# Kernel optimization log

Measured on AMD Instinct MI355X. Metric: run time of the kernel, lower is better.

Reference implementation:

```python
import jax, jax.numpy as jnp
import numpy as np

E, H_HEADS, WS = 512, 16, 8
HEAD_D = E // H_HEADS
LN_EPS = 1e-5


def layernorm(x, g, b):
    mu = jnp.mean(x, axis=-1, keepdims=True)
    var = jnp.mean((x - mu) ** 2, axis=-1, keepdims=True)
    return (x - mu) / jnp.sqrt(var + LN_EPS) * g + b


def setup_inputs() -> dict:
    key = jax.random.key(0)
    ks = jax.random.split(key, 10)
    s = 0.02
    return {
        "x": jax.random.normal(ks[0], (4, 4096, E), jnp.float32),
        "in_proj_w": jax.random.normal(ks[1], (3 * E, E), jnp.float32) * s,
        "in_proj_b": jnp.zeros((3 * E,), jnp.float32),
        "out_w": jax.random.normal(ks[2], (E, E), jnp.float32) * s,
        "out_b": jnp.zeros((E,), jnp.float32),
        "ln1_g": jnp.ones((E,), jnp.float32),
        "ln1_b": jnp.zeros((E,), jnp.float32),
        "w1": jax.random.normal(ks[3], (4 * E, E), jnp.float32) * s,
        "b1": jnp.zeros((4 * E,), jnp.float32),
        "w2": jax.random.normal(ks[4], (E, 4 * E), jnp.float32) * s,
        "b2": jnp.zeros((E,), jnp.float32),
        "ln2_g": jnp.ones((E,), jnp.float32),
        "ln2_b": jnp.zeros((E,), jnp.float32),
        "num_patches_h": 64,
        "num_patches_w": 64,
    }


def reference(x, in_proj_w, in_proj_b, out_w, out_b, ln1_g, ln1_b,
              w1, b1, w2, b2, ln2_g, ln2_b, num_patches_h, num_patches_w):
    B, P, _ = x.shape
    Hp, Wp = num_patches_h, num_patches_w  # 64 divisible by WS -> no padding branch
    nwh, nww = Hp // WS, Wp // WS
    # window partition: (B, Hp, Wp, E) -> (B*nW, WS*WS, E)
    xw = x.reshape(B, nwh, WS, nww, WS, E).transpose(0, 1, 3, 2, 4, 5)
    xw = xw.reshape(B * nwh * nww, WS * WS, E)
    # nn.MultiheadAttention default batch_first=False: axis0 is SEQ (L=B*nW),
    # axis1 is BATCH (N=WS*WS). Reproduce that literal semantics.
    L, N = xw.shape[0], xw.shape[1]
    qkv = xw @ in_proj_w.T + in_proj_b          # (L, N, 3E)
    q, k, v = jnp.split(qkv, 3, axis=-1)
    qh = q.reshape(L, N, H_HEADS, HEAD_D)
    kh = k.reshape(L, N, H_HEADS, HEAD_D)
    vh = v.reshape(L, N, H_HEADS, HEAD_D)
    scale = 1.0 / np.sqrt(HEAD_D)
    scores = jnp.einsum('lnhd,mnhd->nhlm', qh, kh) * scale  # (N, h, L, L)
    attn = jax.nn.softmax(scores, axis=-1)
    o = jnp.einsum('nhlm,mnhd->lnhd', attn, vh).reshape(L, N, E)
    attn_out = o @ out_w.T + out_b
    y = layernorm(xw + attn_out, ln1_g, ln1_b)
    ffn = jax.nn.gelu(y @ w1.T + b1, approximate=False) @ w2.T + b2
    y = layernorm(y + ffn, ln2_g, ln2_b)
    # window unpartition
    y = y.reshape(B, nwh, nww, WS, WS, E).transpose(0, 1, 3, 2, 4, 5)
    return y.reshape(B, Hp * Wp, E)[:, :P, :]
```

## Files before the change

### kernel.cpp

```cpp
#include <hip/hip_runtime.h>
#include <cmath>


typedef _Float16 half8 __attribute__((ext_vector_type(8)));
typedef _Float16 half4v __attribute__((ext_vector_type(4)));
typedef float f32x4 __attribute__((ext_vector_type(4)));

#define GLOBAL_AS(p) ((const __attribute__((address_space(1))) void*)(p))
#define LDS_AS(p) ((__attribute__((address_space(3))) void*)(p))

__device__ __forceinline__ void gload_lds16(const _Float16* g, _Float16* l) {
  __builtin_amdgcn_global_load_lds(GLOBAL_AS(g), LDS_AS(l), 16, 0, 0);
}

__device__ __forceinline__ float wave_sum(float v) {
#pragma unroll
  for (int off = 32; off > 0; off >>= 1) v += __shfl_xor(v, off, 64);
  return v;
}

__device__ __forceinline__ float gelu_fast(float x) {
  const float y = 1.5957691216057308f * (x + 0.044715f * x * x * x);
  const float e = __expf(y);
  const float t = 1.0f - 2.0f / (e + 1.0f);
  return 0.5f * x * (1.0f + t);
}

__global__ __launch_bounds__(256) void pre_kernel(
    const float* __restrict__ x, _Float16* __restrict__ xw,
    const float* __restrict__ s0, _Float16* __restrict__ d0,
    const float* __restrict__ s1, _Float16* __restrict__ d1,
    const float* __restrict__ s2, _Float16* __restrict__ d2,
    const float* __restrict__ s3, _Float16* __restrict__ d3) {
  int b = blockIdx.x;
  if (b < 4096) {
    const int idx = b * 256 + threadIdx.x;
    const int t = idx >> 6;
    const int e0 = (idx & 63) << 3;
    const int l = t >> 6, n = t & 63;
    const int bb = l >> 6, wh = (l >> 3) & 7, ww = l & 7;
    const int pi = n >> 3, pj = n & 7;
    const int xrow = (bb * 4096 + (wh * 8 + pi) * 64 + (ww * 8 + pj)) * 512;
    const float4 a = *(const float4*)&x[xrow + e0];
    const float4 c = *(const float4*)&x[xrow + e0 + 4];
    half8 o;
    o[0] = (_Float16)a.x; o[1] = (_Float16)a.y; o[2] = (_Float16)a.z; o[3] = (_Float16)a.w;
    o[4] = (_Float16)c.x; o[5] = (_Float16)c.y; o[6] = (_Float16)c.z; o[7] = (_Float16)c.w;
    *(half8*)&xw[t * 512 + e0] = o;
    return;
  }
  b -= 4096;
  const float* s; _Float16* d;
  if (b < 768) { s = s0; d = d0; }
  else if (b < 1024) { s = s1; d = d1; b -= 768; }
  else if (b < 2048) { s = s2; d = d2; b -= 1024; }
  else { s = s3; d = d3; b -= 2048; }
  const int i = (b * 256 + threadIdx.x) * 4;
  const float4 v = *(const float4*)&s[i];
  half4v o;
  o[0] = (_Float16)v.x; o[1] = (_Float16)v.y; o[2] = (_Float16)v.z; o[3] = (_Float16)v.w;
  *(half4v*)&d[i] = o;
}

template <int EPI, int K, int BN, int MREP>
__global__ __launch_bounds__(256, 4) void gemml_kernel(
    const _Float16* __restrict__ A, const _Float16* __restrict__ B,
    const float* __restrict__ bias, _Float16* __restrict__ C, int N) {
  constexpr int NT = K / 64;
  constexpr int NWR = (BN == 128) ? 2 : 4;
  constexpr int BM = NWR * MREP * 16;
  constexpr int TA = BM * 64;
  constexpr int TB = BN * 64;
  __shared__ _Float16 L[TA + TB];

  const int tid = threadIdx.x, lane = tid & 63, wave = tid >> 6;
  const int wr = (BN == 128) ? (wave >> 1) : wave;
  const int wc = (BN == 128) ? (wave & 1) : 0;
  const int lr = lane & 15, g = lane >> 4;

  const int nbn = N / BN;
  const int cpx = gridDim.x >> 3;
  const int wg = (blockIdx.x & 7) * cpx + (blockIdx.x >> 3);
  const int bm = wg / nbn, bn = wg % nbn;

  const int scol = ((lane & 7) ^ (lane >> 3)) << 3;
  const int srow = lane >> 3;
  const _Float16* aS = A + (size_t)(bm * BM + wave * 8 + srow) * K + scol;
  const _Float16* bS = B + (size_t)(bn * BN + wave * 8 + srow) * K + scol;

  const int sw0 = ((g ^ (lr & 7)) << 3);
  const int sw1 = (((4 + g) ^ (lr & 7)) << 3);
  int arow[MREP], brow[4];
#pragma unroll
  for (int m = 0; m < MREP; ++m) arow[m] = (wr * (MREP * 16) + m * 16 + lr) * 64;
#pragma unroll
  for (int n = 0; n < 4; ++n) brow[n] = TA + (wc * 64 + n * 16 + lr) * 64;

  f32x4 acc[MREP][4] = {};

#pragma unroll 8
  for (int t = 0; t < NT; ++t) {
    const int koff = t * 64;
#pragma unroll
    for (int i = 0; i < BM / 32; ++i)
      gload_lds16(aS + (size_t)(i * 32) * K + koff, &L[(i * 32 + wave * 8) * 64]);
#pragma unroll
    for (int i = 0; i < BN / 32; ++i)
      gload_lds16(bS + (size_t)(i * 32) * K + koff, &L[TA + (i * 32 + wave * 8) * 64]);
    __syncthreads();
    half8 af[MREP], bf[4];
#pragma unroll
    for (int m = 0; m < MREP; ++m) af[m] = *(const half8*)&L[arow[m] + sw0];
#pragma unroll
    for (int n = 0; n < 4; ++n) bf[n] = *(const half8*)&L[brow[n] + sw0];
    __builtin_amdgcn_s_setprio(1);
#pragma unroll
    for (int m = 0; m < MREP; ++m)
#pragma unroll
      for (int n = 0; n < 4; ++n)
        acc[m][n] = __builtin_amdgcn_mfma_f32_16x16x32_f16(af[m], bf[n], acc[m][n], 0, 0, 0);
    __builtin_amdgcn_s_setprio(0);
#pragma unroll
    for (int m = 0; m < MREP; ++m) af[m] = *(const half8*)&L[arow[m] + sw1];
#pragma unroll
    for (int n = 0; n < 4; ++n) bf[n] = *(const half8*)&L[brow[n] + sw1];
    __builtin_amdgcn_s_setprio(1);
#pragma unroll
    for (int m = 0; m < MREP; ++m)
#pragma unroll
      for (int n = 0; n < 4; ++n)
        acc[m][n] = __builtin_amdgcn_mfma_f32_16x16x32_f16(af[m], bf[n], acc[m][n], 0, 0, 0);
    __builtin_amdgcn_s_setprio(0);
    __syncthreads();
  }

  float bsv[4];
#pragma unroll
  for (int n = 0; n < 4; ++n) bsv[n] = bias[bn * BN + wc * 64 + n * 16 + lr];
  _Float16* Lc = &L[0] + wave * (MREP * 16 * 64);
#pragma unroll
  for (int m = 0; m < MREP; ++m)
#pragma unroll
    for (int n = 0; n < 4; ++n)
#pragma unroll
      for (int r = 0; r < 4; ++r) {
        float v = acc[m][n][r] + bsv[n];
        if (EPI == 1) v = gelu_fast(v);
        const int row = m * 16 + g * 4 + r;
        const int col = n * 16 + lr;
        Lc[row * 64 + (col ^ ((row & 7) << 3))] = (_Float16)v;
      }
  asm volatile("s_waitcnt lgkmcnt(0)" ::: "memory");
  const int rrow = lane >> 3, slot = lane & 7;
  const int growb = bm * BM + wr * (MREP * 16);
  const int gcol = bn * BN + wc * 64 + slot * 8;
#pragma unroll
  for (int blk = 0; blk < MREP * 2; ++blk) {
    const int row = blk * 8 + rrow;
    const half8 vv = *(const half8*)&Lc[row * 64 + ((slot ^ (row & 7)) << 3)];
    *(half8*)&C[(size_t)(growb + row) * N + gcol] = vv;
  }
}

__global__ __launch_bounds__(256) void attn_kernel(const _Float16* __restrict__ qkv,
                                                   _Float16* __restrict__ o_out) {
  const int n = blockIdx.x & 63;
  const int h = blockIdx.x >> 6;
  __shared__ _Float16 Ksh[256 * 40];
  __shared__ _Float16 Vt[32 * 264];
  __shared__ _Float16 Pw[4 * 64 * 72];
  const int tid = threadIdx.x;
  const int wq = tid >> 6, lane = tid & 63;
  const int lr = lane & 15, g = lane >> 4;
  const int hq = h * 32;

#pragma unroll
  for (int pass = 0; pass < 4; ++pass) {
    const int e = pass * 2048 + tid * 8;
    const int m = e >> 5, d = e & 31;
    const int base = (m * 64 + n) * 1536 + hq;
    const half8 k8 = *(const half8*)&qkv[base + 512 + d];
    const half8 v8 = *(const half8*)&qkv[base + 1024 + d];
    *(half8*)&Ksh[m * 40 + d] = k8;
#pragma unroll
    for (int j = 0; j < 8; ++j) Vt[(d + j) * 264 + m] = v8[j];
  }
  half8 qf[4];
#pragma unroll
  for (int qt = 0; qt < 4; ++qt) {
    const int qg = wq * 64 + qt * 16 + lr;
    qf[qt] = *(const half8*)&qkv[(qg * 64 + n) * 1536 + hq + g * 8];
  }
  __syncthreads();

  f32x4 o[4][2] = {};
  float den[4] = {0.f, 0.f, 0.f, 0.f};
  const float scale = 0.17677669529663687f;
  _Float16* P = &Pw[wq * (64 * 72)];

  for (int it = 0; it < 4; ++it) {
    const int k0 = it * 64;
#pragma unroll
    for (int qt = 0; qt < 4; ++qt) {
#pragma unroll
      for (int kt = 0; kt < 4; ++kt) {
        const half8 kf = *(const half8*)&Ksh[(k0 + kt * 16 + lr) * 40 + g * 8];
        const f32x4 z = {0.f, 0.f, 0.f, 0.f};
        f32x4 st = __builtin_amdgcn_mfma_f32_16x16x32_f16(kf, qf[qt], z, 0, 0, 0);
        const float p0 = __expf(st[0] * scale);
        const float p1 = __expf(st[1] * scale);
        const float p2 = __expf(st[2] * scale);
        const float p3 = __expf(st[3] * scale);
        den[qt] += (p0 + p1) + (p2 + p3);
        half4v w;
        w[0] = (_Float16)p0; w[1] = (_Float16)p1;
        w[2] = (_Float16)p2; w[3] = (_Float16)p3;
        *(half4v*)&P[(qt * 16 + lr) * 72 + kt * 16 + g * 4] = w;
      }
    }
    __syncthreads();
#pragma unroll
    for (int qt = 0; qt < 4; ++qt) {
#pragma unroll
      for (int ks = 0; ks < 2; ++ks) {
        const half8 pf = *(const half8*)&P[(qt * 16 + lr) * 72 + ks * 32 + g * 8];
#pragma unroll
        for (int dt = 0; dt < 2; ++dt) {
          const half8 vf = *(const half8*)&Vt[(dt * 16 + lr) * 264 + k0 + ks * 32 + g * 8];
          o[qt][dt] = __builtin_amdgcn_mfma_f32_16x16x32_f16(pf, vf, o[qt][dt], 0, 0, 0);
        }
      }
    }
    __syncthreads();
  }

#pragma unroll
  for (int qt = 0; qt < 4; ++qt) {
    float dq = den[qt];
    dq += __shfl_xor(dq, 16);
    dq += __shfl_xor(dq, 32);
    const float inv = 1.0f / dq;
#pragma unroll
    for (int r = 0; r < 4; ++r) {
      const float invr = __shfl(inv, g * 4 + r);
      const int qg = wq * 64 + qt * 16 + g * 4 + r;
      const int obase = (qg * 64 + n) * 512 + hq;
#pragma unroll
      for (int dt = 0; dt < 2; ++dt)
        o_out[obase + dt * 16 + lr] = (_Float16)(o[qt][dt][r] * invr);
    }
  }
}

template <int FINAL>
__global__ __launch_bounds__(256) void ln_kernel(
    const float* __restrict__ res32, const _Float16* __restrict__ res16,
    const _Float16* __restrict__ add16,
    const float* __restrict__ g, const float* __restrict__ b,
    float* __restrict__ out32, _Float16* __restrict__ out16) {
  const int t = blockIdx.x * 4 + (threadIdx.x >> 6);
  const int lane = threadIdx.x & 63;
  const int e0 = lane << 3;
  const int l = t >> 6, n = t & 63;
  const int bb = l >> 6, wh = (l >> 3) & 7, ww = l & 7;
  const int pi = n >> 3, pj = n & 7;
  const int xrow = (bb * 4096 + (wh * 8 + pi) * 64 + (ww * 8 + pj)) * 512;
  const int trow = t * 512;
  const half8 a8 = *(const half8*)&add16[trow + e0];
  float v[8];
  if (FINAL) {
    const half8 r8 = *(const half8*)&res16[trow + e0];
#pragma unroll
    for (int e = 0; e < 8; ++e) v[e] = (float)r8[e] + (float)a8[e];
  } else {
    const float4 ra = *(const float4*)&res32[xrow + e0];
    const float4 rb = *(const float4*)&res32[xrow + e0 + 4];
    v[0] = ra.x + (float)a8[0]; v[1] = ra.y + (float)a8[1];
    v[2] = ra.z + (float)a8[2]; v[3] = ra.w + (float)a8[3];
    v[4] = rb.x + (float)a8[4]; v[5] = rb.y + (float)a8[5];
    v[6] = rb.z + (float)a8[6]; v[7] = rb.w + (float)a8[7];
  }
  float sm = 0.f;
#pragma unroll
  for (int e = 0; e < 8; ++e) sm += v[e];
  sm = wave_sum(sm);
  const float mu = sm * (1.0f / 512.0f);
  float vs = 0.f;
#pragma unroll
  for (int e = 0; e < 8; ++e) { const float d = v[e] - mu; vs += d * d; }
  vs = wave_sum(vs);
  const float rstd = rsqrtf(vs * (1.0f / 512.0f) + 1e-5f);
  const float4 g1 = *(const float4*)&g[e0];
  const float4 g2 = *(const float4*)&g[e0 + 4];
  const float4 b1 = *(const float4*)&b[e0];
  const float4 b2 = *(const float4*)&b[e0 + 4];
  float y[8];
  y[0] = (v[0] - mu) * rstd * g1.x + b1.x; y[1] = (v[1] - mu) * rstd * g1.y + b1.y;
  y[2] = (v[2] - mu) * rstd * g1.z + b1.z; y[3] = (v[3] - mu) * rstd * g1.w + b1.w;
  y[4] = (v[4] - mu) * rstd * g2.x + b2.x; y[5] = (v[5] - mu) * rstd * g2.y + b2.y;
  y[6] = (v[6] - mu) * rstd * g2.z + b2.z; y[7] = (v[7] - mu) * rstd * g2.w + b2.w;
  if (FINAL) {
    *(float4*)&out32[xrow + e0] = make_float4(y[0], y[1], y[2], y[3]);
    *(float4*)&out32[xrow + e0 + 4] = make_float4(y[4], y[5], y[6], y[7]);
  } else {
    half8 o16;
#pragma unroll
    for (int e = 0; e < 8; ++e) o16[e] = (_Float16)y[e];
    *(half8*)&out16[trow + e0] = o16;
  }
}

extern "C" void kernel_launch(void* const* d_in, const int* in_sizes, int n_in,
                              void* d_out, int out_size, void* d_ws, size_t ws_size,
                              hipStream_t stream) {
  const float* x    = (const float*)d_in[0];
  const float* ipw  = (const float*)d_in[1];
  const float* ipb  = (const float*)d_in[2];
  const float* outw = (const float*)d_in[3];
  const float* outb = (const float*)d_in[4];
  const float* ln1g = (const float*)d_in[5];
  const float* ln1b = (const float*)d_in[6];
  const float* w1   = (const float*)d_in[7];
  const float* b1   = (const float*)d_in[8];
  const float* w2   = (const float*)d_in[9];
  const float* b2   = (const float*)d_in[10];
  const float* ln2g = (const float*)d_in[11];
  const float* ln2b = (const float*)d_in[12];
  float* out = (float*)d_out;
  char* ws = (char*)d_ws;

  _Float16* wqkv_h = (_Float16*)(ws + 0);
  _Float16* wout_h = (_Float16*)(ws + 1572864);
  _Float16* w1_h   = (_Float16*)(ws + 2097152);
  _Float16* w2_h   = (_Float16*)(ws + 4194304);
  _Float16* xw_h   = (_Float16*)(ws + 6291456);
  _Float16* qkv_h  = (_Float16*)(ws + 23068672);
  _Float16* attn_h = (_Float16*)(ws + 90177536);
  _Float16* ao_h   = (_Float16*)(ws + 106954752);
  _Float16* h_h = qkv_h;
  _Float16* f_h = attn_h;
  _Float16* y16 = xw_h;

  pre_kernel<<<7168, 256, 0, stream>>>(x, xw_h, ipw, wqkv_h, outw, wout_h,
                                       w1, w1_h, w2, w2_h);
  gemml_kernel<0, 512, 128, 4><<<1536, 256, 0, stream>>>(xw_h, wqkv_h, ipb, qkv_h, 1536);
  attn_kernel<<<1024, 256, 0, stream>>>(qkv_h, attn_h);
  gemml_kernel<0, 512, 64, 2><<<1024, 256, 0, stream>>>(attn_h, wout_h, outb, ao_h, 512);
  ln_kernel<0><<<4096, 256, 0, stream>>>(x, nullptr, ao_h, ln1g, ln1b, nullptr, y16);
  gemml_kernel<1, 512, 128, 4><<<2048, 256, 0, stream>>>(y16, w1_h, b1, h_h, 2048);
  gemml_kernel<0, 2048, 64, 4><<<512, 256, 0, stream>>>(h_h, w2_h, b2, f_h, 512);
  ln_kernel<1><<<4096, 256, 0, stream>>>(nullptr, y16, f_h, ln2g, ln2b, out, nullptr);
}
```

Before: 202.2 us.

## Add double-buffered LDS GEMM with swizzled epilogue for QKV and FFN1

Introduces a new 128x128 tile GEMM kernel that double-buffers A/B tiles in LDS via direct global-to-LDS loads, prefetching the next K tile while MFMAs run on the current one. It raises wave priority around the MFMA bursts and stages outputs through swizzled LDS for coalesced 16-byte stores. It replaces the previous GEMM for the QKV projection and the first FFN layer. The larger LDS footprint lowers occupancy to 2 blocks per CU, trading latency hiding by occupancy for intra-block overlap.

Result: no change. 205.3 us (+1.5%).

```diff
diff --git a/kernel.cpp b/kernel.cpp
--- a/kernel.cpp
+++ b/kernel.cpp
@@ -62,6 +62,114 @@
   *(half4v*)&d[i] = o;
 }
 
+template <int EPI, int K>
+__global__ __launch_bounds__(256, 2) void gemmd_kernel(
+    const _Float16* __restrict__ A, const _Float16* __restrict__ B,
+    const float* __restrict__ bias, _Float16* __restrict__ C, int N) {
+  constexpr int NT = K / 64;
+  constexpr int TA = 128 * 64;
+  constexpr int TT = 2 * TA;
+  __shared__ _Float16 L[2][TT];
+
+  const int tid = threadIdx.x, lane = tid & 63, wave = tid >> 6;
+  const int wr = wave >> 1, wc = wave & 1;
+  const int lr = lane & 15, g = lane >> 4;
+
+  const int nbn = N >> 7;
+  const int cpx = gridDim.x >> 3;
+  const int wg = (blockIdx.x & 7) * cpx + (blockIdx.x >> 3);
+  const int bm = wg / nbn, bn = wg % nbn;
+
+  const int scol = ((lane & 7) ^ (lane >> 3)) << 3;
+  const int srow = lane >> 3;
+  const _Float16* aS = A + (size_t)(bm * 128 + wave * 8 + srow) * K + scol;
+  const _Float16* bS = B + (size_t)(bn * 128 + wave * 8 + srow) * K + scol;
+
+  auto stage = [&](int b, int t) {
+    const int koff = t * 64;
+#pragma unroll
+    for (int i = 0; i < 4; ++i)
+      gload_lds16(aS + (size_t)(i * 32) * K + koff, &L[b][(i * 32 + wave * 8) * 64]);
+#pragma unroll
+    for (int i = 0; i < 4; ++i)
+      gload_lds16(bS + (size_t)(i * 32) * K + koff, &L[b][TA + (i * 32 + wave * 8) * 64]);
+  };
+
+  const int sw0 = ((g ^ (lr & 7)) << 3);
+  const int sw1 = (((4 + g) ^ (lr & 7)) << 3);
+  int arow[4], brow[4];
+#pragma unroll
+  for (int m = 0; m < 4; ++m) arow[m] = (wr * 64 + m * 16 + lr) * 64;
+#pragma unroll
+  for (int n = 0; n < 4; ++n) brow[n] = TA + (wc * 64 + n * 16 + lr) * 64;
+
+  f32x4 acc[4][4] = {};
+
+  stage(0, 0);
+  asm volatile("s_waitcnt vmcnt(0)" ::: "memory");
+  asm volatile("s_barrier" ::: "memory");
+
+#pragma unroll 8
+  for (int t = 0; t < NT; ++t) {
+    const int p = t & 1;
+    if (t + 1 < NT) stage(p ^ 1, t + 1);
+    const _Float16* Lp = &L[p][0];
+    half8 af[4], bf[4];
+#pragma unroll
+    for (int m = 0; m < 4; ++m) af[m] = *(const half8*)&Lp[arow[m] + sw0];
+#pragma unroll
+    for (int n = 0; n < 4; ++n) bf[n] = *(const half8*)&Lp[brow[n] + sw0];
+    __builtin_amdgcn_s_setprio(1);
+#pragma unroll
+    for (int m = 0; m < 4; ++m)
+#pragma unroll
+      for (int n = 0; n < 4; ++n)
+        acc[m][n] = __builtin_amdgcn_mfma_f32_16x16x32_f16(af[m], bf[n], acc[m][n], 0, 0, 0);
+    __builtin_amdgcn_s_setprio(0);
+#pragma unroll
+    for (int m = 0; m < 4; ++m) af[m] = *(const half8*)&Lp[arow[m] + sw1];
+#pragma unroll
+    for (int n = 0; n < 4; ++n) bf[n] = *(const half8*)&Lp[brow[n] + sw1];
+    __builtin_amdgcn_s_setprio(1);
+#pragma unroll
+    for (int m = 0; m < 4; ++m)
+#pragma unroll
+      for (int n = 0; n < 4; ++n)
+        acc[m][n] = __builtin_amdgcn_mfma_f32_16x16x32_f16(af[m], bf[n], acc[m][n], 0, 0, 0);
+    __builtin_amdgcn_s_setprio(0);
+    asm volatile("s_waitcnt lgkmcnt(0)" ::: "memory");
+    asm volatile("s_waitcnt vmcnt(0)" ::: "memory");
+    asm volatile("s_barrier" ::: "memory");
+  }
+
+  float bsv[4];
+#pragma unroll
+  for (int n = 0; n < 4; ++n) bsv[n] = bias[bn * 128 + wc * 64 + n * 16 + lr];
+  _Float16* Lc = &L[0][0] + wave * 4096;
+#pragma unroll
+  for (int m = 0; m < 4; ++m)
+#pragma unroll
+    for (int n = 0; n < 4; ++n)
+#pragma unroll
+      for (int r = 0; r < 4; ++r) {
+        float v = acc[m][n][r] + bsv[n];
+        if (EPI == 1) v = gelu_fast(v);
+        const int row = m * 16 + g * 4 + r;
+        const int col = n * 16 + lr;
+        Lc[row * 64 + (col ^ ((row & 7) << 3))] = (_Float16)v;
+      }
+  asm volatile("s_waitcnt lgkmcnt(0)" ::: "memory");
+  const int rrow = lane >> 3, slot = lane & 7;
+  const int growb = bm * 128 + wr * 64;
+  const int gcol = bn * 128 + wc * 64 + slot * 8;
+#pragma unroll
+  for (int blk = 0; blk < 8; ++blk) {
+    const int row = blk * 8 + rrow;
+    const half8 vv = *(const half8*)&Lc[row * 64 + ((slot ^ (row & 7)) << 3)];
+    *(half8*)&C[(size_t)(growb + row) * N + gcol] = vv;
+  }
+}
+
 template <int EPI, int K, int BN, int MREP>
 __global__ __launch_bounds__(256, 4) void gemml_kernel(
     const _Float16* __restrict__ A, const _Float16* __restrict__ B,
@@ -343,11 +451,11 @@
 
   pre_kernel<<<7168, 256, 0, stream>>>(x, xw_h, ipw, wqkv_h, outw, wout_h,
                                        w1, w1_h, w2, w2_h);
-  gemml_kernel<0, 512, 128, 4><<<1536, 256, 0, stream>>>(xw_h, wqkv_h, ipb, qkv_h, 1536);
+  gemmd_kernel<0, 512><<<1536, 256, 0, stream>>>(xw_h, wqkv_h, ipb, qkv_h, 1536);
   attn_kernel<<<1024, 256, 0, stream>>>(qkv_h, attn_h);
   gemml_kernel<0, 512, 64, 2><<<1024, 256, 0, stream>>>(attn_h, wout_h, outb, ao_h, 512);
   ln_kernel<0><<<4096, 256, 0, stream>>>(x, nullptr, ao_h, ln1g, ln1b, nullptr, y16);
-  gemml_kernel<1, 512, 128, 4><<<2048, 256, 0, stream>>>(y16, w1_h, b1, h_h, 2048);
+  gemmd_kernel<1, 512><<<2048, 256, 0, stream>>>(y16, w1_h, b1, h_h, 2048);
   gemml_kernel<0, 2048, 64, 4><<<512, 256, 0, stream>>>(h_h, w2_h, b2, f_h, 512);
   ln_kernel<1><<<4096, 256, 0, stream>>>(nullptr, y16, f_h, ln2g, ln2b, out, nullptr);
 }
```
